# Kernel tuning notes

Measured on AMD Instinct MI355X. Metric: run time of the kernel, lower is better.

The kernel has to match this reference:

```python
import jax, jax.numpy as jnp
import numpy as np

B = 4096        # batch_size
D = 128         # embedding dim
TEMP = 0.5      # temperature
EPS = 1e-8      # torch CosineSimilarity eps


def _mask_indices(batch_size):
    """Static flat indices replicating torch boolean-mask (row-major) gather."""
    n = 2 * batch_size
    pos = np.eye(n, n, k=batch_size, dtype=np.float64)
    tril = np.tril(np.ones((n, n), dtype=np.float64))
    neg = (1.0 - tril - pos).astype(bool)
    pos_idx = np.flatnonzero(pos.astype(bool).ravel())
    neg_idx = np.flatnonzero(neg.ravel())
    return jnp.asarray(pos_idx), jnp.asarray(neg_idx)

_POS_IDX, _NEG_IDX = _mask_indices(B)


def setup_inputs() -> dict:
    key = jax.random.key(0)
    k1, k2 = jax.random.split(key)
    zis = jax.random.normal(k1, (B, D), dtype=jnp.float32)
    zjs = jax.random.normal(k2, (B, D), dtype=jnp.float32)
    return {"zis": zis, "zjs": zjs}


def reference(zis, zjs):
    # representations = cat([zjs, zis])  -> [2B, D]
    reps = jnp.concatenate([zjs, zis], axis=0)
    # cosine similarity matrix via normalize + GEMM (same math as broadcasted CosineSimilarity)
    norm = jnp.sqrt(jnp.sum(reps * reps, axis=-1, keepdims=True))
    nreps = reps / jnp.maximum(norm, EPS)
    sim = nreps @ nreps.T                      # [2B, 2B]
    flat = sim.reshape(-1)
    positives = flat[_POS_IDX].reshape(B, -1)  # [B, 1]
    negatives = flat[_NEG_IDX].reshape(B, -1)  # [B, 2B-2]
    logits = jnp.concatenate([positives, negatives], axis=1) / TEMP  # [B, 2B-1]
    # CrossEntropy with labels all zero, reduction='sum'
    logp = jax.nn.log_softmax(logits, axis=-1)
    loss = -jnp.sum(logp[:, 0])
    return loss / B
```

## Files before the change

kernel.cpp:

```cpp
#include <hip/hip_runtime.h>
#include <hip/hip_bf16.h>
#include <math.h>

#define B_  4096u
#define N_  8192
#define D_  128
#define M_  8190u
#define SB_ 25159680u
#define NT2_ 1056

#define AS1 __attribute__((address_space(1)))
#define AS3 __attribute__((address_space(3)))

typedef __attribute__((ext_vector_type(8))) short bf16x8;
typedef __attribute__((ext_vector_type(4))) float f32x4;
typedef __attribute__((ext_vector_type(4))) short short4v;

static __device__ __forceinline__ short f2b(float x) {
  __hip_bfloat16 h = __float2bfloat16(x);
  union { __hip_bfloat16 h; short s; } u; u.h = h; return u.s;
}
static __device__ __forceinline__ unsigned rowS(unsigned i) {
  if (i <= B_) return i * (2u * B_ - 2u) - (i * (i - 1u)) / 2u;
  unsigned d = i - B_;
  return SB_ + d * (B_ - 1u) - (d * (d - 1u)) / 2u;
}
static __device__ __forceinline__ int tile0(int m) {
  return 32 * m - (m * m - 2 * m + (m & 1)) / 4;
}
template <int CTRL>
static __device__ __forceinline__ float dpp_add(float x) {
  union { float f; int i; } u, r;
  u.f = x;
  r.i = __builtin_amdgcn_mov_dpp(u.i, CTRL, 0xF, 0xF, 0);
  return x + r.f;
}
static __device__ __forceinline__ float rsum16(float x) {
  x = dpp_add<0x121>(x);
  x = dpp_add<0x122>(x);
  x = dpp_add<0x124>(x);
  x = dpp_add<0x128>(x);
  return x;
}

__global__ __launch_bounds__(256) void nt_norm(
    const float* __restrict__ zis, const float* __restrict__ zjs,
    short* __restrict__ nb, unsigned* __restrict__ Trow,
    unsigned* __restrict__ zbase) {
  const int t   = threadIdx.x;
  const int row = blockIdx.x * 8 + (t >> 5);
  const int c   = t & 31;
  const float* src = (row < (int)B_) ? (zjs + (size_t)row * D_)
                                     : (zis + (size_t)(row - (int)B_) * D_);
  float4 v = *(const float4*)(src + c * 4);
  float s = v.x * v.x + v.y * v.y + v.z * v.z + v.w * v.w;
  #pragma unroll
  for (int m = 16; m >= 1; m >>= 1) s += __shfl_xor(s, m, 32);
  float rn = 1.0f / fmaxf(sqrtf(s), 1e-8f);
  short4v o;
  o[0] = f2b(v.x * rn); o[1] = f2b(v.y * rn);
  o[2] = f2b(v.z * rn); o[3] = f2b(v.w * rn);
  *(short4v*)(nb + (size_t)row * D_ + c * 4) = o;

  if (t < 8) {
    unsigned i   = (unsigned)(blockIdx.x * 8 + t);
    unsigned S   = rowS(i);
    unsigned rlo = S / M_;
    unsigned Sh  = (rlo + 1u) * M_;
    unsigned jt  = Sh - S + i + 1u;
    Trow[i] = jt + ((i < B_ && jt > i + B_) ? 1u : 0u);
  }
  if (blockIdx.x == 0) {
    for (int r = t; r < 4128; r += 256) zbase[r] = 0u;
  }
}

__global__ __launch_bounds__(512, 4) void nt_gemm(
    const short* __restrict__ nb, const unsigned* __restrict__ Trow,
    float2* __restrict__ part, float* __restrict__ posl) {
  const int tb = ((int)blockIdx.x & 7) * 132 + ((int)blockIdx.x >> 3);
  int bi2 = (int)(2.0f * (32.0f - sqrtf(fmaxf(0.f, 1024.0f - (float)tb))));
  if (bi2 > 63) bi2 = 63;
  while (bi2 > 0 && tb < tile0(bi2)) --bi2;
  while (tb >= tile0(bi2 + 1)) ++bi2;
  const int jlo = bi2 >> 1;
  const int bj2 = jlo + (tb - tile0(bi2));

  __shared__ short As[2][128 * 32];
  __shared__ short Bs[2][256 * 32];
  __shared__ float2 red2[4][128];

  const int t    = threadIdx.x;
  const int lane = t & 63, wave = t >> 6;
  const int li   = lane & 15, hi = lane >> 4;
  const int wr   = wave >> 2, wc = wave & 3;
  const int i0   = bi2 * 128, j0 = bj2 * 256;

  const short* gA = nb + (size_t)i0 * D_;
  const short* gB = nb + (size_t)j0 * D_;

#define STAGE(ko, buf) do {                                                   \
    { int e_ = t; int r_ = e_ >> 2, sl_ = e_ & 3, sg_ = sl_ ^ ((r_ >> 1) & 3);\
      __builtin_amdgcn_global_load_lds(                                       \
          (const AS1 void*)(gA + (size_t)r_ * D_ + (ko) + sg_ * 8),           \
          (AS3 void*)(&As[buf][e_ * 8]), 16, 0, 0); }                         \
    _Pragma("unroll")                                                         \
    for (int it_ = 0; it_ < 2; ++it_) {                                       \
      int e_ = it_ * 512 + t;                                                 \
      int r_ = e_ >> 2, sl_ = e_ & 3, sg_ = sl_ ^ ((r_ >> 1) & 3);            \
      __builtin_amdgcn_global_load_lds(                                       \
          (const AS1 void*)(gB + (size_t)r_ * D_ + (ko) + sg_ * 8),           \
          (AS3 void*)(&Bs[buf][e_ * 8]), 16, 0, 0); }                         \
  } while (0)

  STAGE(0, 0);

  f32x4 acc[4][4];
  #pragma unroll
  for (int m = 0; m < 4; ++m)
    #pragma unroll
    for (int n = 0; n < 4; ++n) acc[m][n] = (f32x4){0.f, 0.f, 0.f, 0.f};

  const int sw = hi ^ ((li >> 1) & 3);

  #pragma unroll
  for (int ph = 0; ph < 4; ++ph) {
    asm volatile("s_waitcnt vmcnt(0)" ::: "memory");
    __builtin_amdgcn_s_barrier();
    __builtin_amdgcn_sched_barrier(0);

    if (ph < 3) STAGE((ph + 1) * 32, (ph + 1) & 1);

    const int cb = ph & 1;
    bf16x8 af[4], bfr[4];
    #pragma unroll
    for (int m = 0; m < 4; ++m)
      af[m] = *(const bf16x8*)(&As[cb][(wr * 64 + m * 16 + li) * 32 + sw * 8]);
    #pragma unroll
    for (int n = 0; n < 4; ++n)
      bfr[n] = *(const bf16x8*)(&Bs[cb][(wc * 64 + n * 16 + li) * 32 + sw * 8]);
    #pragma unroll
    for (int m = 0; m < 4; ++m)
      #pragma unroll
      for (int n = 0; n < 4; ++n)
        acc[m][n] = __builtin_amdgcn_mfma_f32_16x16x32_bf16(
            af[m], bfr[n], acc[m][n], 0, 0, 0);
  }
#undef STAGE

  const bool isdiag = (bj2 == jlo);
  const bool ispost = (bj2 == jlo + 16);
  const bool special = isdiag | ispost;
  const unsigned jw0 = (unsigned)(j0 + wc * 64);

  #pragma unroll
  for (int m = 0; m < 4; ++m) {
    const uint4 T4 = *(const uint4*)(Trow + i0 + wr * 64 + m * 16 + hi * 4);
    const unsigned Ts[4] = {T4.x, T4.y, T4.z, T4.w};
    #pragma unroll
    for (int rg = 0; rg < 4; ++rg) {
      const unsigned i = (unsigned)(i0 + wr * 64 + m * 16 + hi * 4 + rg);
      const unsigned T = Ts[rg];
      float r0, r1;
      if (special) {
        float s0 = 0.f, s1 = 0.f;
        #pragma unroll
        for (int n = 0; n < 4; ++n) {
          const unsigned j = jw0 + n * 16 + (unsigned)li;
          const bool ip = ispost && (j == i + B_);
          if (ip) posl[i] = 2.0f * acc[m][n][rg];
          if ((j > i) && !ip) {
            float e = __expf(2.0f * acc[m][n][rg]);
            if (j < T) s0 += e; else s1 += e;
          }
        }
        r0 = rsum16(s0); r1 = rsum16(s1);
      } else if ((T > jw0) && (T < jw0 + 64u)) {
        float s0 = 0.f, s1 = 0.f;
        #pragma unroll
        for (int n = 0; n < 4; ++n) {
          const unsigned j = jw0 + n * 16 + (unsigned)li;
          float e = __expf(2.0f * acc[m][n][rg]);
          if (j < T) s0 += e; else s1 += e;
        }
        r0 = rsum16(s0); r1 = rsum16(s1);
      } else {
        float s = 0.f;
        #pragma unroll
        for (int n = 0; n < 4; ++n) s += __expf(2.0f * acc[m][n][rg]);
        s = rsum16(s);
        const bool lo = (T > jw0);
        r0 = lo ? s : 0.f;
        r1 = lo ? 0.f : s;
      }
      if (li == 0)
        red2[wc][wr * 64 + m * 16 + hi * 4 + rg] = make_float2(r0, r1);
    }
  }
  __syncthreads();

  if (t < 128) {
    float2 s = make_float2(0.f, 0.f);
    #pragma unroll
    for (int w = 0; w < 4; ++w) {
      float2 v = red2[w][t];
      s.x += v.x; s.y += v.y;
    }
    part[(size_t)tb * 128 + t] = s;
  }
}

__global__ __launch_bounds__(256) void nt_rowfin(
    const float2* __restrict__ part, const float* __restrict__ posl,
    float* __restrict__ E, unsigned* __restrict__ counter,
    float* __restrict__ out) {
  __shared__ float2 xch[128];
  __shared__ int lastflag;
  __shared__ double red[256];
  const int bi2 = (int)blockIdx.x;
  const int t = threadIdx.x;
  const int lrow = t & 127, sh = t >> 7;
  const int base = tile0(bi2);
  const int cnt  = 32 - (bi2 >> 1);

  float2 s = make_float2(0.f, 0.f);
  for (int c = sh; c < cnt; c += 2) {
    float2 v = part[(size_t)(base + c) * 128 + lrow];
    s.x += v.x; s.y += v.y;
  }
  if (sh == 1) xch[lrow] = s;
  __syncthreads();
  if (sh == 0) {
    float2 v = xch[lrow];
    s.x += v.x; s.y += v.y;
    const unsigned i   = (unsigned)(bi2 * 128 + lrow);
    const unsigned rlo = rowS(i) / M_;
    atomicAdd(&E[rlo],      s.x);
    atomicAdd(&E[rlo + 1u], s.y);
  }
  __threadfence();
  __syncthreads();
  if (t == 0) lastflag = (atomicAdd(counter, 1u) == 63u) ? 1 : 0;
  __syncthreads();
  if (!lastflag) return;

  __threadfence();
  double acc = 0.0;
  for (int r = t; r < (int)B_; r += 256) {
    float ev = atomicAdd(&E[r], 0.0f);
    float pl = posl[r];
    acc += (double)(logf(__expf(pl) + ev) - pl);
  }
  red[t] = acc;
  __syncthreads();
  for (int m = 128; m > 0; m >>= 1) {
    if (t < m) red[t] += red[t + m];
    __syncthreads();
  }
  if (t == 0) out[0] = (float)(red[0] / (double)B_);
}

extern "C" void kernel_launch(void* const* d_in, const int* in_sizes, int n_in,
                              void* d_out, int out_size, void* d_ws, size_t ws_size,
                              hipStream_t stream) {
  const float* zis = (const float*)d_in[0];
  const float* zjs = (const float*)d_in[1];
  float* out = (float*)d_out;

  char* ws = (char*)d_ws;
  short*    nb      = (short*)ws;
  unsigned* Trow    = (unsigned*)(ws + 2097152);
  float*    posl    = (float*)(ws + 2129920);
  float2*   part    = (float2*)(ws + 2146304);
  float*    E       = (float*)(ws + 3227648);
  unsigned* counter = (unsigned*)(ws + 3244096);
  unsigned* zb      = (unsigned*)E;

  nt_norm  <<<dim3(N_ / 8), 256, 0, stream>>>(zis, zjs, nb, Trow, zb);
  nt_gemm  <<<dim3(NT2_),   512, 0, stream>>>(nb, Trow, part, posl);
  nt_rowfin<<<dim3(64),     256, 0, stream>>>(part, posl, E, counter, out);
}
```

Before: 55.02 us.

## Process two tiles per GEMM block with cross-tile prefetch and inline row thresholds

```diff
diff --git a/kernel.cpp b/kernel.cpp
--- a/kernel.cpp
+++ b/kernel.cpp
@@ -8,6 +8,7 @@
 #define M_  8190u
 #define SB_ 25159680u
 #define NT2_ 1056
+#define NBLK 528
 
 #define AS1 __attribute__((address_space(1)))
 #define AS3 __attribute__((address_space(3)))
@@ -45,8 +46,7 @@
 
 __global__ __launch_bounds__(256) void nt_norm(
     const float* __restrict__ zis, const float* __restrict__ zjs,
-    short* __restrict__ nb, unsigned* __restrict__ Trow,
-    unsigned* __restrict__ zbase) {
+    short* __restrict__ nb, unsigned* __restrict__ zbase) {
   const int t   = threadIdx.x;
   const int row = blockIdx.x * 8 + (t >> 5);
   const int c   = t & 31;
@@ -62,29 +62,22 @@
   o[2] = f2b(v.z * rn); o[3] = f2b(v.w * rn);
   *(short4v*)(nb + (size_t)row * D_ + c * 4) = o;
 
-  if (t < 8) {
-    unsigned i   = (unsigned)(blockIdx.x * 8 + t);
-    unsigned S   = rowS(i);
-    unsigned rlo = S / M_;
-    unsigned Sh  = (rlo + 1u) * M_;
-    unsigned jt  = Sh - S + i + 1u;
-    Trow[i] = jt + ((i < B_ && jt > i + B_) ? 1u : 0u);
-  }
   if (blockIdx.x == 0) {
     for (int r = t; r < 4128; r += 256) zbase[r] = 0u;
   }
 }
 
 __global__ __launch_bounds__(512, 4) void nt_gemm(
-    const short* __restrict__ nb, const unsigned* __restrict__ Trow,
-    float2* __restrict__ part, float* __restrict__ posl) {
-  const int tb = ((int)blockIdx.x & 7) * 132 + ((int)blockIdx.x >> 3);
-  int bi2 = (int)(2.0f * (32.0f - sqrtf(fmaxf(0.f, 1024.0f - (float)tb))));
+    const short* __restrict__ nb, float2* __restrict__ part,
+    float* __restrict__ posl) {
+  const int tb0 = (int)blockIdx.x * 2;
+  int bi2 = (int)(2.0f * (32.0f - sqrtf(fmaxf(0.f, 1024.0f - (float)tb0))));
   if (bi2 > 63) bi2 = 63;
-  while (bi2 > 0 && tb < tile0(bi2)) --bi2;
-  while (tb >= tile0(bi2 + 1)) ++bi2;
-  const int jlo = bi2 >> 1;
-  const int bj2 = jlo + (tb - tile0(bi2));
+  while (bi2 > 0 && tb0 < tile0(bi2)) --bi2;
+  while (tb0 >= tile0(bi2 + 1)) ++bi2;
+  int bj2 = (bi2 >> 1) + (tb0 - tile0(bi2));
+  int bi2b = bi2, bj2b = bj2 + 1;
+  if (bj2b >= 32) { bi2b = bi2 + 1; bj2b = bi2b >> 1; }
 
   __shared__ short As[2][128 * 32];
   __shared__ short Bs[2][256 * 32];
@@ -94,26 +87,29 @@
   const int lane = t & 63, wave = t >> 6;
   const int li   = lane & 15, hi = lane >> 4;
   const int wr   = wave >> 2, wc = wave & 3;
-  const int i0   = bi2 * 128, j0 = bj2 * 256;
-
-  const short* gA = nb + (size_t)i0 * D_;
-  const short* gB = nb + (size_t)j0 * D_;
-
-#define STAGE(ko, buf) do {                                                   \
+  const int i0a  = bi2 * 128,  j0a = bj2 * 256;
+  const int i0b  = bi2b * 128, j0b = bj2b * 256;
+
+  const short* gA0 = nb + (size_t)i0a * D_;
+  const short* gB0 = nb + (size_t)j0a * D_;
+  const short* gA1 = nb + (size_t)i0b * D_;
+  const short* gB1 = nb + (size_t)j0b * D_;
+
+#define STAGE(gAp, gBp, ko, buf) do {                                         \
     { int e_ = t; int r_ = e_ >> 2, sl_ = e_ & 3, sg_ = sl_ ^ ((r_ >> 1) & 3);\
       __builtin_amdgcn_global_load_lds(                                       \
-          (const AS1 void*)(gA + (size_t)r_ * D_ + (ko) + sg_ * 8),           \
+          (const AS1 void*)((gAp) + (size_t)r_ * D_ + (ko) + sg_ * 8),        \
           (AS3 void*)(&As[buf][e_ * 8]), 16, 0, 0); }                         \
     _Pragma("unroll")                                                         \
     for (int it_ = 0; it_ < 2; ++it_) {                                       \
       int e_ = it_ * 512 + t;                                                 \
       int r_ = e_ >> 2, sl_ = e_ & 3, sg_ = sl_ ^ ((r_ >> 1) & 3);            \
       __builtin_amdgcn_global_load_lds(                                       \
-          (const AS1 void*)(gB + (size_t)r_ * D_ + (ko) + sg_ * 8),           \
+          (const AS1 void*)((gBp) + (size_t)r_ * D_ + (ko) + sg_ * 8),        \
           (AS3 void*)(&Bs[buf][e_ * 8]), 16, 0, 0); }                         \
   } while (0)
 
-  STAGE(0, 0);
+  STAGE(gA0, gB0, 0, 0);
 
   f32x4 acc[4][4];
   #pragma unroll
@@ -124,14 +120,18 @@
   const int sw = hi ^ ((li >> 1) & 3);
 
   #pragma unroll
-  for (int ph = 0; ph < 4; ++ph) {
+  for (int s = 0; s < 8; ++s) {
     asm volatile("s_waitcnt vmcnt(0)" ::: "memory");
     __builtin_amdgcn_s_barrier();
     __builtin_amdgcn_sched_barrier(0);
 
-    if (ph < 3) STAGE((ph + 1) * 32, (ph + 1) & 1);
-
-    const int cb = ph & 1;
+    if (s < 7) {
+      const short* gAn = ((s + 1) >> 2) ? gA1 : gA0;
+      const short* gBn = ((s + 1) >> 2) ? gB1 : gB0;
+      STAGE(gAn, gBn, ((s + 1) & 3) * 32, (s + 1) & 1);
+    }
+
+    const int cb = s & 1;
     bf16x8 af[4], bfr[4];
     #pragma unroll
     for (int m = 0; m < 4; ++m)
@@ -145,78 +145,90 @@
       for (int n = 0; n < 4; ++n)
         acc[m][n] = __builtin_amdgcn_mfma_f32_16x16x32_bf16(
             af[m], bfr[n], acc[m][n], 0, 0, 0);
+
+    if ((s & 3) == 3) {
+      const int  ti0  = (s >> 2) ? i0b : i0a;
+      const int  tj0  = (s >> 2) ? j0b : j0a;
+      const int  tbi2 = (s >> 2) ? bi2b : bi2;
+      const int  tbj2 = (s >> 2) ? bj2b : bj2;
+      const int  ttb  = tb0 + (s >> 2);
+      const int  jlo_t = tbi2 >> 1;
+      const bool isdiag = (tbj2 == jlo_t);
+      const bool ispost = (tbj2 == jlo_t + 16);
+      const bool special = isdiag | ispost;
+      const unsigned jw0 = (unsigned)(tj0 + wc * 64);
+
+      #pragma unroll
+      for (int m = 0; m < 4; ++m) {
+        #pragma unroll
+        for (int rg = 0; rg < 4; ++rg) {
+          const unsigned i = (unsigned)(ti0 + wr * 64 + m * 16 + hi * 4 + rg);
+          const unsigned S = rowS(i);
+          unsigned T = (S / M_ + 1u) * M_ - S + i + 1u;
+          T += ((i < B_) && (T > i + B_)) ? 1u : 0u;
+          float r0, r1;
+          if (special) {
+            float s0 = 0.f, s1 = 0.f;
+            #pragma unroll
+            for (int n = 0; n < 4; ++n) {
+              const unsigned j = jw0 + n * 16 + (unsigned)li;
+              const bool ip = ispost && (j == i + B_);
+              if (ip) posl[i] = 2.0f * acc[m][n][rg];
+              if ((j > i) && !ip) {
+                float e = __expf(2.0f * acc[m][n][rg]);
+                if (j < T) s0 += e; else s1 += e;
+              }
+            }
+            r0 = rsum16(s0); r1 = rsum16(s1);
+          } else if ((T > jw0) && (T < jw0 + 64u)) {
+            float s0 = 0.f, s1 = 0.f;
+            #pragma unroll
+            for (int n = 0; n < 4; ++n) {
+              const unsigned j = jw0 + n * 16 + (unsigned)li;
+              float e = __expf(2.0f * acc[m][n][rg]);
+              if (j < T) s0 += e; else s1 += e;
+            }
+            r0 = rsum16(s0); r1 = rsum16(s1);
+          } else {
+            float sv = 0.f;
+            #pragma unroll
+            for (int n = 0; n < 4; ++n) sv += __expf(2.0f * acc[m][n][rg]);
+            sv = rsum16(sv);
+            const bool lo = (T > jw0);
+            r0 = lo ? sv : 0.f;
+            r1 = lo ? 0.f : sv;
+          }
+          if (li == 0)
+            red2[wc][wr * 64 + m * 16 + hi * 4 + rg] = make_float2(r0, r1);
+        }
+      }
+      asm volatile("s_waitcnt lgkmcnt(0)" ::: "memory");
+      __builtin_amdgcn_s_barrier();
+      if (t < 128) {
+        float2 sm = make_float2(0.f, 0.f);
+        #pragma unroll
+        for (int w = 0; w < 4; ++w) {
+          float2 v = red2[w][t];
+          sm.x += v.x; sm.y += v.y;
+        }
+        part[(size_t)ttb * 128 + t] = sm;
+      }
+      #pragma unroll
+      for (int m = 0; m < 4; ++m)
+        #pragma unroll
+        for (int n = 0; n < 4; ++n) acc[m][n] = (f32x4){0.f, 0.f, 0.f, 0.f};
+    }
   }
 #undef STAGE
-
-  const bool isdiag = (bj2 == jlo);
-  const bool ispost = (bj2 == jlo + 16);
-  const bool special = isdiag | ispost;
-  const unsigned jw0 = (unsigned)(j0 + wc * 64);
-
-  #pragma unroll
-  for (int m = 0; m < 4; ++m) {
-    const uint4 T4 = *(const uint4*)(Trow + i0 + wr * 64 + m * 16 + hi * 4);
-    const unsigned Ts[4] = {T4.x, T4.y, T4.z, T4.w};
-    #pragma unroll
-    for (int rg = 0; rg < 4; ++rg) {
-      const unsigned i = (unsigned)(i0 + wr * 64 + m * 16 + hi * 4 + rg);
-      const unsigned T = Ts[rg];
-      float r0, r1;
-      if (special) {
-        float s0 = 0.f, s1 = 0.f;
-        #pragma unroll
-        for (int n = 0; n < 4; ++n) {
-          const unsigned j = jw0 + n * 16 + (unsigned)li;
-          const bool ip = ispost && (j == i + B_);
-          if (ip) posl[i] = 2.0f * acc[m][n][rg];
-          if ((j > i) && !ip) {
-            float e = __expf(2.0f * acc[m][n][rg]);
-            if (j < T) s0 += e; else s1 += e;
-          }
-        }
-        r0 = rsum16(s0); r1 = rsum16(s1);
-      } else if ((T > jw0) && (T < jw0 + 64u)) {
-        float s0 = 0.f, s1 = 0.f;
-        #pragma unroll
-        for (int n = 0; n < 4; ++n) {
-          const unsigned j = jw0 + n * 16 + (unsigned)li;
-          float e = __expf(2.0f * acc[m][n][rg]);
-          if (j < T) s0 += e; else s1 += e;
-        }
-        r0 = rsum16(s0); r1 = rsum16(s1);
-      } else {
-        float s = 0.f;
-        #pragma unroll
-        for (int n = 0; n < 4; ++n) s += __expf(2.0f * acc[m][n][rg]);
-        s = rsum16(s);
-        const bool lo = (T > jw0);
-        r0 = lo ? s : 0.f;
-        r1 = lo ? 0.f : s;
-      }
-      if (li == 0)
-        red2[wc][wr * 64 + m * 16 + hi * 4 + rg] = make_float2(r0, r1);
-    }
-  }
-  __syncthreads();
-
-  if (t < 128) {
-    float2 s = make_float2(0.f, 0.f);
-    #pragma unroll
-    for (int w = 0; w < 4; ++w) {
-      float2 v = red2[w][t];
-      s.x += v.x; s.y += v.y;
-    }
-    part[(size_t)tb * 128 + t] = s;
-  }
-}
-
-__global__ __launch_bounds__(256) void nt_rowfin(
+}
+
+__global__ __launch_bounds__(1024) void nt_rowfin(
     const float2* __restrict__ part, const float* __restrict__ posl,
     float* __restrict__ E, unsigned* __restrict__ counter,
     float* __restrict__ out) {
-  __shared__ float2 xch[128];
+  __shared__ float2 xch[8][128];
   __shared__ int lastflag;
-  __shared__ double red[256];
+  __shared__ double red[1024];
   const int bi2 = (int)blockIdx.x;
   const int t = threadIdx.x;
   const int lrow = t & 127, sh = t >> 7;
@@ -224,19 +236,23 @@
   const int cnt  = 32 - (bi2 >> 1);
 
   float2 s = make_float2(0.f, 0.f);
-  for (int c = sh; c < cnt; c += 2) {
+  for (int c = sh; c < cnt; c += 8) {
     float2 v = part[(size_t)(base + c) * 128 + lrow];
     s.x += v.x; s.y += v.y;
   }
-  if (sh == 1) xch[lrow] = s;
-  __syncthreads();
-  if (sh == 0) {
-    float2 v = xch[lrow];
-    s.x += v.x; s.y += v.y;
-    const unsigned i   = (unsigned)(bi2 * 128 + lrow);
+  xch[sh][lrow] = s;
+  __syncthreads();
+  if (t < 128) {
+    float sx = 0.f, sy = 0.f;
+    #pragma unroll
+    for (int w = 0; w < 8; ++w) {
+      float2 v = xch[w][t];
+      sx += v.x; sy += v.y;
+    }
+    const unsigned i   = (unsigned)(bi2 * 128 + t);
     const unsigned rlo = rowS(i) / M_;
-    atomicAdd(&E[rlo],      s.x);
-    atomicAdd(&E[rlo + 1u], s.y);
+    atomicAdd(&E[rlo],      sx);
+    atomicAdd(&E[rlo + 1u], sy);
   }
   __threadfence();
   __syncthreads();
@@ -246,14 +262,14 @@
 
   __threadfence();
   double acc = 0.0;
-  for (int r = t; r < (int)B_; r += 256) {
+  for (int r = t; r < (int)B_; r += 1024) {
     float ev = atomicAdd(&E[r], 0.0f);
     float pl = posl[r];
     acc += (double)(logf(__expf(pl) + ev) - pl);
   }
   red[t] = acc;
   __syncthreads();
-  for (int m = 128; m > 0; m >>= 1) {
+  for (int m = 512; m > 0; m >>= 1) {
     if (t < m) red[t] += red[t + m];
     __syncthreads();
   }
@@ -269,14 +285,13 @@
 
   char* ws = (char*)d_ws;
   short*    nb      = (short*)ws;
-  unsigned* Trow    = (unsigned*)(ws + 2097152);
-  float*    posl    = (float*)(ws + 2129920);
-  float2*   part    = (float2*)(ws + 2146304);
-  float*    E       = (float*)(ws + 3227648);
-  unsigned* counter = (unsigned*)(ws + 3244096);
+  float*    posl    = (float*)(ws + 2097152);
+  float2*   part    = (float2*)(ws + 2113536);
+  float*    E       = (float*)(ws + 3194880);
+  unsigned* counter = (unsigned*)(ws + 3211328);
   unsigned* zb      = (unsigned*)E;
 
-  nt_norm  <<<dim3(N_ / 8), 256, 0, stream>>>(zis, zjs, nb, Trow, zb);
-  nt_gemm  <<<dim3(NT2_),   512, 0, stream>>>(nb, Trow, part, posl);
-  nt_rowfin<<<dim3(64),     256, 0, stream>>>(part, posl, E, counter, out);
-}
+  nt_norm  <<<dim3(N_ / 8), 256, 0, stream>>>(zis, zjs, nb, zb);
+  nt_gemm  <<<dim3(NBLK),   512, 0, stream>>>(nb, part, posl);
+  nt_rowfin<<<dim3(64),     1024, 0, stream>>>(part, posl, E, counter, out);
+}
```

New measurement: 71.31 us. 29.6% more time.

## Drop in-block LDS reduction in GEMM epilogue and recompute row thresholds inline

Applied to the files above, without the earlier changes.

```diff
diff --git a/kernel.cpp b/kernel.cpp
--- a/kernel.cpp
+++ b/kernel.cpp
@@ -45,8 +45,7 @@
 
 __global__ __launch_bounds__(256) void nt_norm(
     const float* __restrict__ zis, const float* __restrict__ zjs,
-    short* __restrict__ nb, unsigned* __restrict__ Trow,
-    unsigned* __restrict__ zbase) {
+    short* __restrict__ nb, unsigned* __restrict__ zbase) {
   const int t   = threadIdx.x;
   const int row = blockIdx.x * 8 + (t >> 5);
   const int c   = t & 31;
@@ -62,22 +61,14 @@
   o[2] = f2b(v.z * rn); o[3] = f2b(v.w * rn);
   *(short4v*)(nb + (size_t)row * D_ + c * 4) = o;
 
-  if (t < 8) {
-    unsigned i   = (unsigned)(blockIdx.x * 8 + t);
-    unsigned S   = rowS(i);
-    unsigned rlo = S / M_;
-    unsigned Sh  = (rlo + 1u) * M_;
-    unsigned jt  = Sh - S + i + 1u;
-    Trow[i] = jt + ((i < B_ && jt > i + B_) ? 1u : 0u);
-  }
   if (blockIdx.x == 0) {
     for (int r = t; r < 4128; r += 256) zbase[r] = 0u;
   }
 }
 
 __global__ __launch_bounds__(512, 4) void nt_gemm(
-    const short* __restrict__ nb, const unsigned* __restrict__ Trow,
-    float2* __restrict__ part, float* __restrict__ posl) {
+    const short* __restrict__ nb, float2* __restrict__ part,
+    float* __restrict__ posl) {
   const int tb = ((int)blockIdx.x & 7) * 132 + ((int)blockIdx.x >> 3);
   int bi2 = (int)(2.0f * (32.0f - sqrtf(fmaxf(0.f, 1024.0f - (float)tb))));
   if (bi2 > 63) bi2 = 63;
@@ -88,7 +79,6 @@
 
   __shared__ short As[2][128 * 32];
   __shared__ short Bs[2][256 * 32];
-  __shared__ float2 red2[4][128];
 
   const int t    = threadIdx.x;
   const int lane = t & 63, wave = t >> 6;
@@ -139,12 +129,14 @@
     #pragma unroll
     for (int n = 0; n < 4; ++n)
       bfr[n] = *(const bf16x8*)(&Bs[cb][(wc * 64 + n * 16 + li) * 32 + sw * 8]);
+    __builtin_amdgcn_s_setprio(1);
     #pragma unroll
     for (int m = 0; m < 4; ++m)
       #pragma unroll
       for (int n = 0; n < 4; ++n)
         acc[m][n] = __builtin_amdgcn_mfma_f32_16x16x32_bf16(
             af[m], bfr[n], acc[m][n], 0, 0, 0);
+    __builtin_amdgcn_s_setprio(0);
   }
 #undef STAGE
 
@@ -152,15 +144,17 @@
   const bool ispost = (bj2 == jlo + 16);
   const bool special = isdiag | ispost;
   const unsigned jw0 = (unsigned)(j0 + wc * 64);
+  float2* pw = part + ((size_t)tb * 4 + wc) * 128;
 
   #pragma unroll
   for (int m = 0; m < 4; ++m) {
-    const uint4 T4 = *(const uint4*)(Trow + i0 + wr * 64 + m * 16 + hi * 4);
-    const unsigned Ts[4] = {T4.x, T4.y, T4.z, T4.w};
     #pragma unroll
     for (int rg = 0; rg < 4; ++rg) {
-      const unsigned i = (unsigned)(i0 + wr * 64 + m * 16 + hi * 4 + rg);
-      const unsigned T = Ts[rg];
+      const int lrow = wr * 64 + m * 16 + hi * 4 + rg;
+      const unsigned i = (unsigned)(i0 + lrow);
+      const unsigned S = rowS(i);
+      unsigned T = (S / M_ + 1u) * M_ - S + i + 1u;
+      T += ((i < B_) && (T > i + B_)) ? 1u : 0u;
       float r0, r1;
       if (special) {
         float s0 = 0.f, s1 = 0.f;
@@ -193,50 +187,42 @@
         r0 = lo ? s : 0.f;
         r1 = lo ? 0.f : s;
       }
-      if (li == 0)
-        red2[wc][wr * 64 + m * 16 + hi * 4 + rg] = make_float2(r0, r1);
+      if (li == 0) pw[lrow] = make_float2(r0, r1);
     }
   }
-  __syncthreads();
-
-  if (t < 128) {
-    float2 s = make_float2(0.f, 0.f);
-    #pragma unroll
-    for (int w = 0; w < 4; ++w) {
-      float2 v = red2[w][t];
-      s.x += v.x; s.y += v.y;
-    }
-    part[(size_t)tb * 128 + t] = s;
-  }
-}
-
-__global__ __launch_bounds__(256) void nt_rowfin(
+}
+
+__global__ __launch_bounds__(1024) void nt_rowfin(
     const float2* __restrict__ part, const float* __restrict__ posl,
     float* __restrict__ E, unsigned* __restrict__ counter,
     float* __restrict__ out) {
-  __shared__ float2 xch[128];
+  __shared__ float2 xch[8][128];
   __shared__ int lastflag;
-  __shared__ double red[256];
+  __shared__ double red[1024];
   const int bi2 = (int)blockIdx.x;
   const int t = threadIdx.x;
   const int lrow = t & 127, sh = t >> 7;
-  const int base = tile0(bi2);
-  const int cnt  = 32 - (bi2 >> 1);
+  const int base4 = tile0(bi2) * 4;
+  const int nsl   = (32 - (bi2 >> 1)) * 4;
 
   float2 s = make_float2(0.f, 0.f);
-  for (int c = sh; c < cnt; c += 2) {
-    float2 v = part[(size_t)(base + c) * 128 + lrow];
+  for (int c = sh; c < nsl; c += 8) {
+    float2 v = part[(size_t)(base4 + c) * 128 + lrow];
     s.x += v.x; s.y += v.y;
   }
-  if (sh == 1) xch[lrow] = s;
-  __syncthreads();
-  if (sh == 0) {
-    float2 v = xch[lrow];
-    s.x += v.x; s.y += v.y;
-    const unsigned i   = (unsigned)(bi2 * 128 + lrow);
+  xch[sh][lrow] = s;
+  __syncthreads();
+  if (t < 128) {
+    float sx = 0.f, sy = 0.f;
+    #pragma unroll
+    for (int w = 0; w < 8; ++w) {
+      float2 v = xch[w][t];
+      sx += v.x; sy += v.y;
+    }
+    const unsigned i   = (unsigned)(bi2 * 128 + t);
     const unsigned rlo = rowS(i) / M_;
-    atomicAdd(&E[rlo],      s.x);
-    atomicAdd(&E[rlo + 1u], s.y);
+    atomicAdd(&E[rlo],      sx);
+    atomicAdd(&E[rlo + 1u], sy);
   }
   __threadfence();
   __syncthreads();
@@ -246,14 +232,14 @@
 
   __threadfence();
   double acc = 0.0;
-  for (int r = t; r < (int)B_; r += 256) {
+  for (int r = t; r < (int)B_; r += 1024) {
     float ev = atomicAdd(&E[r], 0.0f);
     float pl = posl[r];
     acc += (double)(logf(__expf(pl) + ev) - pl);
   }
   red[t] = acc;
   __syncthreads();
-  for (int m = 128; m > 0; m >>= 1) {
+  for (int m = 512; m > 0; m >>= 1) {
     if (t < m) red[t] += red[t + m];
     __syncthreads();
   }
@@ -269,14 +255,13 @@
 
   char* ws = (char*)d_ws;
   short*    nb      = (short*)ws;
-  unsigned* Trow    = (unsigned*)(ws + 2097152);
-  float*    posl    = (float*)(ws + 2129920);
-  float2*   part    = (float2*)(ws + 2146304);
-  float*    E       = (float*)(ws + 3227648);
-  unsigned* counter = (unsigned*)(ws + 3244096);
+  float*    posl    = (float*)(ws + 2097152);
+  float2*   part    = (float2*)(ws + 2113536);
+  float*    E       = (float*)(ws + 6438912);
+  unsigned* counter = (unsigned*)(ws + 6455360);
   unsigned* zb      = (unsigned*)E;
 
-  nt_norm  <<<dim3(N_ / 8), 256, 0, stream>>>(zis, zjs, nb, Trow, zb);
-  nt_gemm  <<<dim3(NT2_),   512, 0, stream>>>(nb, Trow, part, posl);
-  nt_rowfin<<<dim3(64),     256, 0, stream>>>(part, posl, E, counter, out);
-}
+  nt_norm  <<<dim3(N_ / 8), 256, 0, stream>>>(zis, zjs, nb, zb);
+  nt_gemm  <<<dim3(NT2_),   512, 0, stream>>>(nb, part, posl);
+  nt_rowfin<<<dim3(64),     1024, 0, stream>>>(part, posl, E, counter, out);
+}
```

Measured after the change: 68.41 us. 24.3% more time.

## Switch normalized embeddings to FP8 and use scaled MFMA 16x16x128

Applied to the files above, without the earlier changes.

```diff
diff --git a/kernel.cpp b/kernel.cpp
--- a/kernel.cpp
+++ b/kernel.cpp
@@ -12,14 +12,10 @@
 #define AS1 __attribute__((address_space(1)))
 #define AS3 __attribute__((address_space(3)))
 
-typedef __attribute__((ext_vector_type(8))) short bf16x8;
+typedef __attribute__((ext_vector_type(8))) int   i32x8;
+typedef __attribute__((ext_vector_type(4))) int   i32x4;
 typedef __attribute__((ext_vector_type(4))) float f32x4;
-typedef __attribute__((ext_vector_type(4))) short short4v;
-
-static __device__ __forceinline__ short f2b(float x) {
-  __hip_bfloat16 h = __float2bfloat16(x);
-  union { __hip_bfloat16 h; short s; } u; u.h = h; return u.s;
-}
+
 static __device__ __forceinline__ unsigned rowS(unsigned i) {
   if (i <= B_) return i * (2u * B_ - 2u) - (i * (i - 1u)) / 2u;
   unsigned d = i - B_;
@@ -45,7 +41,7 @@
 
 __global__ __launch_bounds__(256) void nt_norm(
     const float* __restrict__ zis, const float* __restrict__ zjs,
-    short* __restrict__ nb, unsigned* __restrict__ Trow,
+    unsigned* __restrict__ nb8, unsigned* __restrict__ Trow,
     unsigned* __restrict__ zbase) {
   const int t   = threadIdx.x;
   const int row = blockIdx.x * 8 + (t >> 5);
@@ -57,10 +53,9 @@
   #pragma unroll
   for (int m = 16; m >= 1; m >>= 1) s += __shfl_xor(s, m, 32);
   float rn = 1.0f / fmaxf(sqrtf(s), 1e-8f);
-  short4v o;
-  o[0] = f2b(v.x * rn); o[1] = f2b(v.y * rn);
-  o[2] = f2b(v.z * rn); o[3] = f2b(v.w * rn);
-  *(short4v*)(nb + (size_t)row * D_ + c * 4) = o;
+  int p = __builtin_amdgcn_cvt_pk_fp8_f32(v.x * rn, v.y * rn, 0, false);
+  p     = __builtin_amdgcn_cvt_pk_fp8_f32(v.z * rn, v.w * rn, p, true);
+  nb8[(size_t)row * 32 + c] = (unsigned)p;
 
   if (t < 8) {
     unsigned i   = (unsigned)(blockIdx.x * 8 + t);
@@ -76,7 +71,7 @@
 }
 
 __global__ __launch_bounds__(512, 4) void nt_gemm(
-    const short* __restrict__ nb, const unsigned* __restrict__ Trow,
+    const char* __restrict__ nb, const unsigned* __restrict__ Trow,
     float2* __restrict__ part, float* __restrict__ posl) {
   const int tb = ((int)blockIdx.x & 7) * 132 + ((int)blockIdx.x >> 3);
   int bi2 = (int)(2.0f * (32.0f - sqrtf(fmaxf(0.f, 1024.0f - (float)tb))));
@@ -86,8 +81,8 @@
   const int jlo = bi2 >> 1;
   const int bj2 = jlo + (tb - tile0(bi2));
 
-  __shared__ short As[2][128 * 32];
-  __shared__ short Bs[2][256 * 32];
+  __shared__ char Asm[128 * 128];
+  __shared__ char Bsm[256 * 128];
   __shared__ float2 red2[4][128];
 
   const int t    = threadIdx.x;
@@ -96,24 +91,23 @@
   const int wr   = wave >> 2, wc = wave & 3;
   const int i0   = bi2 * 128, j0 = bj2 * 256;
 
-  const short* gA = nb + (size_t)i0 * D_;
-  const short* gB = nb + (size_t)j0 * D_;
-
-#define STAGE(ko, buf) do {                                                   \
-    { int e_ = t; int r_ = e_ >> 2, sl_ = e_ & 3, sg_ = sl_ ^ ((r_ >> 1) & 3);\
-      __builtin_amdgcn_global_load_lds(                                       \
-          (const AS1 void*)(gA + (size_t)r_ * D_ + (ko) + sg_ * 8),           \
-          (AS3 void*)(&As[buf][e_ * 8]), 16, 0, 0); }                         \
-    _Pragma("unroll")                                                         \
-    for (int it_ = 0; it_ < 2; ++it_) {                                       \
-      int e_ = it_ * 512 + t;                                                 \
-      int r_ = e_ >> 2, sl_ = e_ & 3, sg_ = sl_ ^ ((r_ >> 1) & 3);            \
-      __builtin_amdgcn_global_load_lds(                                       \
-          (const AS1 void*)(gB + (size_t)r_ * D_ + (ko) + sg_ * 8),           \
-          (AS3 void*)(&Bs[buf][e_ * 8]), 16, 0, 0); }                         \
-  } while (0)
-
-  STAGE(0, 0);
+  const char* gA = nb + (size_t)i0 * 128;
+  const char* gB = nb + (size_t)j0 * 128;
+
+  #pragma unroll
+  for (int it = 0; it < 2; ++it) {
+    int e = it * 512 + t, r = e >> 3, sl = e & 7, sg = sl ^ (r & 7);
+    __builtin_amdgcn_global_load_lds(
+        (const AS1 void*)(gA + (size_t)r * 128 + sg * 16),
+        (AS3 void*)(Asm + e * 16), 16, 0, 0);
+  }
+  #pragma unroll
+  for (int it = 0; it < 4; ++it) {
+    int e = it * 512 + t, r = e >> 3, sl = e & 7, sg = sl ^ (r & 7);
+    __builtin_amdgcn_global_load_lds(
+        (const AS1 void*)(gB + (size_t)r * 128 + sg * 16),
+        (AS3 void*)(Bsm + e * 16), 16, 0, 0);
+  }
 
   f32x4 acc[4][4];
   #pragma unroll
@@ -121,32 +115,37 @@
     #pragma unroll
     for (int n = 0; n < 4; ++n) acc[m][n] = (f32x4){0.f, 0.f, 0.f, 0.f};
 
-  const int sw = hi ^ ((li >> 1) & 3);
-
-  #pragma unroll
-  for (int ph = 0; ph < 4; ++ph) {
-    asm volatile("s_waitcnt vmcnt(0)" ::: "memory");
-    __builtin_amdgcn_s_barrier();
-    __builtin_amdgcn_sched_barrier(0);
-
-    if (ph < 3) STAGE((ph + 1) * 32, (ph + 1) & 1);
-
-    const int cb = ph & 1;
-    bf16x8 af[4], bfr[4];
+  asm volatile("s_waitcnt vmcnt(0)" ::: "memory");
+  __builtin_amdgcn_s_barrier();
+  __builtin_amdgcn_sched_barrier(0);
+
+  i32x8 af[4];
+  #pragma unroll
+  for (int m = 0; m < 4; ++m) {
+    const int R = wr * 64 + m * 16 + li, rb = R & 7;
+    i32x4 lo = *(const i32x4*)(Asm + (size_t)R * 128 + (((hi << 1)    ) ^ rb) * 16);
+    i32x4 hv = *(const i32x4*)(Asm + (size_t)R * 128 + (((hi << 1) | 1) ^ rb) * 16);
+    af[m][0] = lo[0]; af[m][1] = lo[1]; af[m][2] = lo[2]; af[m][3] = lo[3];
+    af[m][4] = hv[0]; af[m][5] = hv[1]; af[m][6] = hv[2]; af[m][7] = hv[3];
+  }
+
+  __builtin_amdgcn_s_setprio(1);
+  #pragma unroll
+  for (int n = 0; n < 4; ++n) {
+    const int R = wc * 64 + n * 16 + li, rb = R & 7;
+    i32x4 lo = *(const i32x4*)(Bsm + (size_t)R * 128 + (((hi << 1)    ) ^ rb) * 16);
+    i32x4 hv = *(const i32x4*)(Bsm + (size_t)R * 128 + (((hi << 1) | 1) ^ rb) * 16);
+    i32x8 bfr;
+    bfr[0] = lo[0]; bfr[1] = lo[1]; bfr[2] = lo[2]; bfr[3] = lo[3];
+    bfr[4] = hv[0]; bfr[5] = hv[1]; bfr[6] = hv[2]; bfr[7] = hv[3];
     #pragma unroll
     for (int m = 0; m < 4; ++m)
-      af[m] = *(const bf16x8*)(&As[cb][(wr * 64 + m * 16 + li) * 32 + sw * 8]);
-    #pragma unroll
-    for (int n = 0; n < 4; ++n)
-      bfr[n] = *(const bf16x8*)(&Bs[cb][(wc * 64 + n * 16 + li) * 32 + sw * 8]);
-    #pragma unroll
-    for (int m = 0; m < 4; ++m)
-      #pragma unroll
-      for (int n = 0; n < 4; ++n)
-        acc[m][n] = __builtin_amdgcn_mfma_f32_16x16x32_bf16(
-            af[m], bfr[n], acc[m][n], 0, 0, 0);
-  }
-#undef STAGE
+      acc[m][n] = __builtin_amdgcn_mfma_scale_f32_16x16x128_f8f6f4(
+          af[m], bfr, acc[m][n], 0, 0,
+          0, 127,
+          0, 127);
+  }
+  __builtin_amdgcn_s_setprio(0);
 
   const bool isdiag = (bj2 == jlo);
   const bool ispost = (bj2 == jlo + 16);
@@ -268,15 +267,15 @@
   float* out = (float*)d_out;
 
   char* ws = (char*)d_ws;
-  short*    nb      = (short*)ws;
-  unsigned* Trow    = (unsigned*)(ws + 2097152);
-  float*    posl    = (float*)(ws + 2129920);
-  float2*   part    = (float2*)(ws + 2146304);
-  float*    E       = (float*)(ws + 3227648);
-  unsigned* counter = (unsigned*)(ws + 3244096);
+  char*     nb      = ws;
+  unsigned* Trow    = (unsigned*)(ws + 1048576);
+  float*    posl    = (float*)(ws + 1081344);
+  float2*   part    = (float2*)(ws + 1097728);
+  float*    E       = (float*)(ws + 2179072);
+  unsigned* counter = (unsigned*)(ws + 2195520);
   unsigned* zb      = (unsigned*)E;
 
-  nt_norm  <<<dim3(N_ / 8), 256, 0, stream>>>(zis, zjs, nb, Trow, zb);
+  nt_norm  <<<dim3(N_ / 8), 256, 0, stream>>>(zis, zjs, (unsigned*)nb, Trow, zb);
   nt_gemm  <<<dim3(NT2_),   512, 0, stream>>>(nb, Trow, part, posl);
   nt_rowfin<<<dim3(64),     256, 0, stream>>>(part, posl, E, counter, out);
 }
```

After: 51.28 us. 1.07x faster.
